# Performance work log

Measured on AMD Instinct MI355X. Metric: run time of the kernel, lower is better.

The kernel has to match this reference:

```python
import jax, jax.numpy as jnp
import numpy as np

NUM_HEADS = 16
HEAD_DIM = 64
ROT_DIM = HEAD_DIM // 2  # RotaryEmbedding(dim=head_dim/2) rotates first 32 dims only
THETA = 10000.0


def _rope(x):
    # x: [b, h, l, d]; interleaved (lucidrains) rotary on first ROT_DIM dims.
    L = x.shape[-2]
    inv_freq = 1.0 / (THETA ** (jnp.arange(0, ROT_DIM, 2, dtype=jnp.float32) / ROT_DIM))  # [ROT_DIM/2]
    ang = jnp.arange(L, dtype=jnp.float32)[:, None] * inv_freq[None, :]  # [l, ROT_DIM/2]
    ang = jnp.repeat(ang, 2, axis=-1)  # [l, ROT_DIM] (each freq repeated for the pair)
    cos, sin = jnp.cos(ang), jnp.sin(ang)
    x_rot, x_pass = x[..., :ROT_DIM], x[..., ROT_DIM:]
    x1 = x_rot[..., 0::2]
    x2 = x_rot[..., 1::2]
    rot_half = jnp.stack([-x2, x1], axis=-1).reshape(x_rot.shape)  # rotate_half, interleaved
    x_rot = x_rot * cos + rot_half * sin
    return jnp.concatenate([x_rot, x_pass], axis=-1)


def setup_inputs() -> dict:
    key = jax.random.key(0)
    ks = jax.random.split(key, 7)
    B, L, E = 2, 2048, 1024
    s = 1.0 / np.sqrt(E)
    return {
        "query": jax.random.normal(ks[0], (B, L, E), jnp.float32),
        "key": jax.random.normal(ks[1], (B, L, E), jnp.float32),
        "value": jax.random.normal(ks[2], (B, L, E), jnp.float32),
        "Wq": jax.random.normal(ks[3], (E, E), jnp.float32) * s,
        "Wk": jax.random.normal(ks[4], (E, E), jnp.float32) * s,
        "Wv": jax.random.normal(ks[5], (E, E), jnp.float32) * s,
        "Wo": jax.random.normal(ks[6], (E, E), jnp.float32) * s,
        "bo": jnp.zeros((E,), jnp.float32),
    }


def reference(query, key, value, Wq, Wk, Wv, Wo, bo):
    B, L, E = query.shape
    H, D = NUM_HEADS, HEAD_DIM
    scaling = D ** (-0.5)

    def split_heads(x):
        return x.reshape(B, L, H, D).transpose(0, 2, 1, 3)  # b h l d

    q = split_heads(query @ Wq.T)
    k = split_heads(key @ Wk.T)
    v = split_heads(value @ Wv.T)
    q = _rope(q)
    k = _rope(k)
    # NOTE: source divides by scaling (multiplies by sqrt(D)) -- faithful to original.
    attn_weight = jnp.einsum('bhid,bhjd->bhij', q, k) / scaling
    # NOTE: softmax over dim=-2 (query axis), as in the original code.
    attn_weight = jax.nn.softmax(attn_weight, axis=-2)
    attn = jnp.einsum('bhij,bhjd->bhid', attn_weight, v)
    attn = attn.transpose(0, 2, 1, 3).reshape(B, L, E)
    out = attn @ Wo.T + bo
    return out, attn_weight
```

## Files before the change

kernel.cpp:

```cpp
#include <hip/hip_runtime.h>
#include <cmath>

typedef __bf16 bf16;
typedef __attribute__((ext_vector_type(4))) __bf16 bf16x4;
typedef __attribute__((ext_vector_type(8))) __bf16 bf16x8;
typedef __attribute__((ext_vector_type(4))) float f32x4;

#define MFMA16(a, b, c) __builtin_amdgcn_mfma_f32_16x16x32_bf16((a), (b), (c), 0, 0, 0)
#define SETPRIO1 __builtin_amdgcn_s_setprio(1)
#define SETPRIO0 __builtin_amdgcn_s_setprio(0)
#define EXP2(x) __builtin_amdgcn_exp2f(x)
#define WAITV_BAR(N) asm volatile("s_waitcnt vmcnt(" #N ")\n\ts_barrier" ::: "memory")
#define WAITL_BAR    asm volatile("s_waitcnt lgkmcnt(0)\n\ts_barrier" ::: "memory")

#define LOG2E 1.4426950408889634f

static __device__ __forceinline__ void gload16(const bf16* g, bf16* l)
{
  __builtin_amdgcn_global_load_lds((const __attribute__((address_space(1))) void*)g,
                                   (__attribute__((address_space(3))) void*)l, 16, 0, 0);
}

static __device__ __forceinline__ void split4(const float4 v, bf16x4& h, bf16x4& l)
{
  h[0] = (bf16)v.x; l[0] = (bf16)(v.x - (float)h[0]);
  h[1] = (bf16)v.y; l[1] = (bf16)(v.y - (float)h[1]);
  h[2] = (bf16)v.z; l[2] = (bf16)(v.z - (float)h[2]);
  h[3] = (bf16)v.w; l[3] = (bf16)(v.w - (float)h[3]);
}

__global__ __launch_bounds__(256) void conv_kernel(
    const float* __restrict__ query, const float* __restrict__ key, const float* __restrict__ value,
    const float* __restrict__ Wq, const float* __restrict__ Wk, const float* __restrict__ Wv,
    const float* __restrict__ Wo,
    bf16* __restrict__ qh, bf16* __restrict__ ql, bf16* __restrict__ kh, bf16* __restrict__ kl,
    bf16* __restrict__ wqh, bf16* __restrict__ wql, bf16* __restrict__ wkh, bf16* __restrict__ wkl,
    bf16* __restrict__ vb, bf16* __restrict__ wvb, bf16* __restrict__ wob)
{
  const int i = blockIdx.x * 256 + threadIdx.x;
  const float* src;
  bf16 *dh, *dl;
  int e;
  if (i < 1048576)      { src = query; dh = qh; dl = ql; e = i; }
  else if (i < 2097152) { src = key;   dh = kh; dl = kl; e = i - 1048576; }
  else if (i < 3145728) { src = value; dh = vb; dl = nullptr; e = i - 2097152; }
  else {
    const int w = i - 3145728;
    const int which = w >> 18;
    e = w & 262143;
    src = (which == 0) ? Wq : (which == 1) ? Wk : (which == 2) ? Wv : Wo;
    dh  = (which == 0) ? wqh : (which == 1) ? wkh : (which == 2) ? wvb : wob;
    dl  = (which == 0) ? wql : (which == 1) ? wkl : nullptr;
  }
  const float4 v = ((const float4*)src)[e];
  bf16x4 h, l;
  split4(v, h, l);
  *(bf16x4*)(dh + (size_t)e * 4) = h;
  if (dl) *(bf16x4*)(dl + (size_t)e * 4) = l;
}

__global__ __launch_bounds__(256) void projqk_kernel(
    const bf16* __restrict__ qh, const bf16* __restrict__ ql,
    const bf16* __restrict__ kh, const bf16* __restrict__ kl,
    const bf16* __restrict__ wqh, const bf16* __restrict__ wql,
    const bf16* __restrict__ wkh, const bf16* __restrict__ wkl,
    bf16* __restrict__ Qh_g, bf16* __restrict__ Ql_g,
    bf16* __restrict__ Kh_g, bf16* __restrict__ Kl_g)
{
  const int which = blockIdx.y;
  const bf16* ta[4];
  ta[0] = which ? kh : qh;   ta[1] = which ? kl : ql;
  ta[2] = which ? wkh : wqh; ta[3] = which ? wkl : wql;
  bf16* oh = which ? Kh_g : Qh_g;
  bf16* ol = which ? Kl_g : Ql_g;
  const float oscale = which ? 8.0f * LOG2E : 1.0f;

  __shared__ __align__(16) bf16 sm[2][4][4096];
  const int tid = threadIdx.x, lane = tid & 63, w = tid >> 6;
  const int wm = w >> 1, wn = w & 1;
  const int fr = lane & 15, fg = lane >> 4;
  const int bm = blockIdx.x >> 3, bn = blockIdx.x & 7;
  const int rb[4] = {bm * 128, bm * 128, bn * 128, bn * 128};
  const int lrow = lane >> 2, lcol = (lane & 3) * 8;

  auto stage = [&](int buf, int kt) {
#pragma unroll
    for (int tl = 0; tl < 4; ++tl)
#pragma unroll
      for (int q = 0; q < 2; ++q) {
        const int r = (q * 4 + w) * 16 + lrow;
        gload16(ta[tl] + (size_t)(rb[tl] + r) * 1024 + kt * 32 + lcol,
                &sm[buf][tl][(q * 4 + w) * 512]);
      }
  };

  f32x4 acc[4][4] = {};
  stage(0, 0);
  for (int kt = 0; kt < 32; ++kt) {
    const int cur = kt & 1;
    if (kt < 31) { stage(cur ^ 1, kt + 1); WAITV_BAR(8); }
    else         { WAITV_BAR(0); }
    bf16x8 afh[4], afl[4], bfh[4], bfl[4];
#pragma unroll
    for (int m = 0; m < 4; ++m) {
      afh[m] = *(bf16x8*)&sm[cur][0][(wm * 64 + m * 16 + fr) * 32 + fg * 8];
      afl[m] = *(bf16x8*)&sm[cur][1][(wm * 64 + m * 16 + fr) * 32 + fg * 8];
    }
#pragma unroll
    for (int n = 0; n < 4; ++n) {
      bfh[n] = *(bf16x8*)&sm[cur][2][(wn * 64 + n * 16 + fr) * 32 + fg * 8];
      bfl[n] = *(bf16x8*)&sm[cur][3][(wn * 64 + n * 16 + fr) * 32 + fg * 8];
    }
    SETPRIO1;
#pragma unroll
    for (int m = 0; m < 4; ++m)
#pragma unroll
      for (int n = 0; n < 4; ++n) {
        acc[m][n] = MFMA16(afh[m], bfh[n], acc[m][n]);
        acc[m][n] = MFMA16(afh[m], bfl[n], acc[m][n]);
        acc[m][n] = MFMA16(afl[m], bfh[n], acc[m][n]);
      }
    SETPRIO0;
    WAITL_BAR;
  }
#pragma unroll
  for (int n = 0; n < 4; ++n) {
    const int d = n * 16 + fr;
    const bool rot = (n < 2);
    const float invf = rot ? exp2f((float)(d >> 1) * (-0.83048202372184059f)) : 0.0f;
    const int odd = d & 1;
    const int col = bn * 128 + wn * 64 + n * 16 + fr;
#pragma unroll
    for (int m = 0; m < 4; ++m)
#pragma unroll
      for (int r4 = 0; r4 < 4; ++r4) {
        const int row = bm * 128 + wm * 64 + m * 16 + fg * 4 + r4;
        float x = acc[m][n][r4];
        const float p = __shfl_xor(x, 1);
        if (rot) {
          float sn, cs;
          sincosf((float)(row & 2047) * invf, &sn, &cs);
          x = odd ? x * cs + p * sn : x * cs - p * sn;
        }
        x *= oscale;
        const bf16 hv = (bf16)x;
        oh[(size_t)row * 1024 + col] = hv;
        ol[(size_t)row * 1024 + col] = (bf16)(x - (float)hv);
      }
  }
}

__global__ __launch_bounds__(256) void projv_kernel(const bf16* __restrict__ vb,
                                                    const bf16* __restrict__ wvb,
                                                    bf16* __restrict__ Vt_g)
{
  __shared__ __align__(16) bf16 sm[2][2][4096];
  const int tid = threadIdx.x, lane = tid & 63, w = tid >> 6;
  const int wm = w >> 1, wn = w & 1;
  const int fr = lane & 15, fg = lane >> 4;
  const int bm = blockIdx.x >> 3, bn = blockIdx.x & 7;
  const int lrow = lane >> 2, lcol = (lane & 3) * 8;

  auto stage = [&](int buf, int kt) {
#pragma unroll
    for (int q = 0; q < 2; ++q) {
      const int r = (q * 4 + w) * 16 + lrow;
      gload16(vb  + (size_t)(bm * 128 + r) * 1024 + kt * 32 + lcol, &sm[buf][0][(q * 4 + w) * 512]);
      gload16(wvb + (size_t)(bn * 128 + r) * 1024 + kt * 32 + lcol, &sm[buf][1][(q * 4 + w) * 512]);
    }
  };

  f32x4 acc[4][4] = {};
  stage(0, 0);
  for (int kt = 0; kt < 32; ++kt) {
    const int cur = kt & 1;
    if (kt < 31) { stage(cur ^ 1, kt + 1); WAITV_BAR(4); }
    else         { WAITV_BAR(0); }
    bf16x8 af[4], bf[4];
#pragma unroll
    for (int m = 0; m < 4; ++m) af[m] = *(bf16x8*)&sm[cur][0][(wm * 64 + m * 16 + fr) * 32 + fg * 8];
#pragma unroll
    for (int n = 0; n < 4; ++n) bf[n] = *(bf16x8*)&sm[cur][1][(wn * 64 + n * 16 + fr) * 32 + fg * 8];
    SETPRIO1;
#pragma unroll
    for (int m = 0; m < 4; ++m)
#pragma unroll
      for (int n = 0; n < 4; ++n) acc[m][n] = MFMA16(af[m], bf[n], acc[m][n]);
    SETPRIO0;
    WAITL_BAR;
  }
#pragma unroll
  for (int m = 0; m < 4; ++m) {
    const int row0 = bm * 128 + wm * 64 + m * 16 + fg * 4;
    const int b = row0 >> 11, l0 = row0 & 2047;
#pragma unroll
    for (int n = 0; n < 4; ++n) {
      const int col = bn * 128 + wn * 64 + n * 16 + fr;
      const int h = col >> 6, d = col & 63;
      bf16x4 pk;
#pragma unroll
      for (int j = 0; j < 4; ++j) pk[j] = (bf16)acc[m][n][j];
      *(bf16x4*)(Vt_g + ((size_t)((b * 16 + h) * 64 + d)) * 2048 + l0) = pk;
    }
  }
}

__global__ __launch_bounds__(256) void out_kernel(const bf16* __restrict__ attnb,
                                                  const bf16* __restrict__ wob,
                                                  const float* __restrict__ bo,
                                                  float* __restrict__ out)
{
  __shared__ __align__(16) bf16 sm[2][2][4096];
  const int tid = threadIdx.x, lane = tid & 63, w = tid >> 6;
  const int wm = w >> 1, wn = w & 1;
  const int fr = lane & 15, fg = lane >> 4;
  const int bm = blockIdx.x >> 3, bn = blockIdx.x & 7;
  const int lrow = lane >> 2, lcol = (lane & 3) * 8;

  auto stage = [&](int buf, int kt) {
#pragma unroll
    for (int q = 0; q < 2; ++q) {
      const int r = (q * 4 + w) * 16 + lrow;
      gload16(attnb + (size_t)(bm * 128 + r) * 1024 + kt * 32 + lcol, &sm[buf][0][(q * 4 + w) * 512]);
      gload16(wob   + (size_t)(bn * 128 + r) * 1024 + kt * 32 + lcol, &sm[buf][1][(q * 4 + w) * 512]);
    }
  };

  f32x4 acc[4][4] = {};
  stage(0, 0);
  for (int kt = 0; kt < 32; ++kt) {
    const int cur = kt & 1;
    if (kt < 31) { stage(cur ^ 1, kt + 1); WAITV_BAR(4); }
    else         { WAITV_BAR(0); }
    bf16x8 af[4], bf[4];
#pragma unroll
    for (int m = 0; m < 4; ++m) af[m] = *(bf16x8*)&sm[cur][0][(wm * 64 + m * 16 + fr) * 32 + fg * 8];
#pragma unroll
    for (int n = 0; n < 4; ++n) bf[n] = *(bf16x8*)&sm[cur][1][(wn * 64 + n * 16 + fr) * 32 + fg * 8];
    SETPRIO1;
#pragma unroll
    for (int m = 0; m < 4; ++m)
#pragma unroll
      for (int n = 0; n < 4; ++n) acc[m][n] = MFMA16(af[m], bf[n], acc[m][n]);
    SETPRIO0;
    WAITL_BAR;
  }
#pragma unroll
  for (int m = 0; m < 4; ++m)
#pragma unroll
    for (int n = 0; n < 4; ++n) {
      const int col = bn * 128 + wn * 64 + n * 16 + fr;
      const float bv = bo[col];
#pragma unroll
      for (int r4 = 0; r4 < 4; ++r4) {
        const int row = bm * 128 + wm * 64 + m * 16 + fg * 4 + r4;
        out[(size_t)row * 1024 + col] = acc[m][n][r4] + bv;
      }
    }
}

__global__ __launch_bounds__(512) void stats_kernel(const bf16* __restrict__ Qh_g, const bf16* __restrict__ Ql_g,
                                                    const bf16* __restrict__ Kh_g, const bf16* __restrict__ Kl_g,
                                                    float* __restrict__ colmax, float* __restrict__ csuminv)
{
  __shared__ __align__(16) bf16 smh[2][8192], sml[2][8192];
  const int swz = (blockIdx.x & 7) * 64 + (blockIdx.x >> 3);
  const int bh = swz >> 4, jb = swz & 15;
  const int b = bh >> 4, h = bh & 15;
  const int t = threadIdx.x, lane = t & 63, w = t >> 6;
  const int fr = lane & 15, fg = lane >> 4;
  const int lr = lane >> 3, lc = lane & 7;

  auto stageQ = [&](int buf, int it) {
#pragma unroll
    for (int q = 0; q < 2; ++q) {
      const int r = (q * 8 + w) * 8 + lr;
      const size_t g = (size_t)(b * 2048 + it * 128 + r) * 1024 + h * 64 + ((lc ^ (r & 7)) * 8);
      gload16(Qh_g + g, &smh[buf][(q * 8 + w) * 512]);
      gload16(Ql_g + g, &sml[buf][(q * 8 + w) * 512]);
    }
  };

#pragma unroll
  for (int q = 0; q < 2; ++q) {
    const int r = (q * 8 + w) * 8 + lr;
    const size_t g = (size_t)(b * 2048 + jb * 128 + r) * 1024 + h * 64 + ((lc ^ (r & 7)) * 8);
    gload16(Kh_g + g, &smh[1][(q * 8 + w) * 512]);
    gload16(Kl_g + g, &sml[1][(q * 8 + w) * 512]);
  }
  stageQ(0, 0);
  WAITV_BAR(4);
  bf16x8 kfh[2], kfl[2];
#pragma unroll
  for (int ks = 0; ks < 2; ++ks) {
    const int rr = w * 16 + fr;
    const int cc = (ks * 32 + fg * 8) ^ ((rr & 7) << 3);
    kfh[ks] = *(bf16x8*)&smh[1][rr * 64 + cc];
    kfl[ks] = *(bf16x8*)&sml[1][rr * 64 + cc];
  }
  WAITL_BAR;

  float rm[4] = {-1e30f, -1e30f, -1e30f, -1e30f};
  float rs[4] = {0.f, 0.f, 0.f, 0.f};
  for (int it = 0; it < 16; ++it) {
    const int cur = it & 1;
    if (it < 15) { stageQ(cur ^ 1, it + 1); WAITV_BAR(4); }
    else         { WAITV_BAR(0); }
    f32x4 acc[8] = {};
    SETPRIO1;
#pragma unroll
    for (int ks = 0; ks < 2; ++ks)
#pragma unroll
      for (int n = 0; n < 8; ++n) {
        const int rr = n * 16 + fr;
        const int cc = (ks * 32 + fg * 8) ^ ((rr & 7) << 3);
        const bf16x8 qf = *(bf16x8*)&smh[cur][rr * 64 + cc];
        const bf16x8 lf = *(bf16x8*)&sml[cur][rr * 64 + cc];
        acc[n] = MFMA16(kfh[ks], qf, acc[n]);
        acc[n] = MFMA16(kfh[ks], lf, acc[n]);
        acc[n] = MFMA16(kfl[ks], qf, acc[n]);
      }
    SETPRIO0;
#pragma unroll
    for (int r4 = 0; r4 < 4; ++r4) {
      const float m = fmaxf(fmaxf(fmaxf(acc[0][r4], acc[1][r4]), fmaxf(acc[2][r4], acc[3][r4])),
                            fmaxf(fmaxf(acc[4][r4], acc[5][r4]), fmaxf(acc[6][r4], acc[7][r4])));
      const float mn = fmaxf(rm[r4], m);
      float ts = 0.f;
#pragma unroll
      for (int n = 0; n < 8; ++n) ts += EXP2(acc[n][r4] - mn);
      rs[r4] = rs[r4] * EXP2(rm[r4] - mn) + ts;
      rm[r4] = mn;
    }
    WAITL_BAR;
  }
#pragma unroll
  for (int r4 = 0; r4 < 4; ++r4) {
    float M = rm[r4];
#pragma unroll
    for (int off = 1; off < 16; off <<= 1) M = fmaxf(M, __shfl_xor(M, off));
    float s = rs[r4] * EXP2(rm[r4] - M);
#pragma unroll
    for (int off = 1; off < 16; off <<= 1) s += __shfl_xor(s, off);
    rm[r4] = M;
    rs[r4] = s;
  }
  if (fr == 0) {
#pragma unroll
    for (int r4 = 0; r4 < 4; ++r4) {
      const int j = jb * 128 + w * 16 + fg * 4 + r4;
      colmax[bh * 2048 + j] = rm[r4];
      csuminv[bh * 2048 + j] = 1.0f / rs[r4];
    }
  }
}

__global__ __launch_bounds__(256) void attn_kernel(const bf16* __restrict__ Qh_g, const bf16* __restrict__ Ql_g,
                                                   const bf16* __restrict__ Kh_g, const bf16* __restrict__ Kl_g,
                                                   const bf16* __restrict__ Vt_g,
                                                   const float* __restrict__ colmax, const float* __restrict__ csuminv,
                                                   float* __restrict__ P, bf16* __restrict__ attnb)
{
  __shared__ __align__(16) unsigned char smem[46080];
  bf16(*Kh)[72] = (bf16(*)[72])smem;
  bf16(*Kl)[72] = (bf16(*)[72])(smem + 9216);
  bf16(*Vt)[72] = (bf16(*)[72])(smem + 18432);
  bf16(*Pb)[72] = (bf16(*)[72])(smem + 27648);
  bf16(*Qh)[72] = (bf16(*)[72])smem;
  bf16(*Ql)[72] = (bf16(*)[72])(smem + 18432);

  const int swz = (blockIdx.x & 7) * 64 + (blockIdx.x >> 3);
  const int bh = swz >> 4, ib = swz & 15;
  const int b = bh >> 4, h = bh & 15;
  const int t = threadIdx.x, lane = t & 63, w = t >> 6;
  const int fr = lane & 15, fg = lane >> 4;

#pragma unroll
  for (int q = 0; q < 4; ++q) {
    const int u = q * 256 + t, r = u >> 3, c8 = (u & 7) * 8;
    const size_t g = (size_t)(b * 2048 + ib * 128 + r) * 1024 + h * 64 + c8;
    *(bf16x8*)&Qh[r][c8] = *(const bf16x8*)(Qh_g + g);
    *(bf16x8*)&Ql[r][c8] = *(const bf16x8*)(Ql_g + g);
  }
  WAITL_BAR;
  bf16x8 qfh[2][2], qfl[2][2];
#pragma unroll
  for (int mf = 0; mf < 2; ++mf)
#pragma unroll
    for (int ks = 0; ks < 2; ++ks) {
      qfh[mf][ks] = *(bf16x8*)&Qh[w * 32 + mf * 16 + fr][ks * 32 + fg * 8];
      qfl[mf][ks] = *(bf16x8*)&Ql[w * 32 + mf * 16 + fr][ks * 32 + fg * 8];
    }

  bf16x8 rKh[2], rKl[2], rV[2];
  auto loadT = [&](int jt1) {
#pragma unroll
    for (int q = 0; q < 2; ++q) {
      const int u = q * 256 + t, r = u >> 3, c8 = (u & 7) * 8;
      const size_t g = (size_t)(b * 2048 + jt1 * 64 + r) * 1024 + h * 64 + c8;
      rKh[q] = *(const bf16x8*)(Kh_g + g);
      rKl[q] = *(const bf16x8*)(Kl_g + g);
      rV[q]  = *(const bf16x8*)(Vt_g + (size_t)(bh * 64 + r) * 2048 + jt1 * 64 + c8);
    }
  };
  auto writeK = [&]() {
#pragma unroll
    for (int q = 0; q < 2; ++q) {
      const int u = q * 256 + t, r = u >> 3, c8 = (u & 7) * 8;
      *(bf16x8*)&Kh[r][c8] = rKh[q];
      *(bf16x8*)&Kl[r][c8] = rKl[q];
    }
  };
  auto writeV = [&]() {
#pragma unroll
    for (int q = 0; q < 2; ++q) {
      const int u = q * 256 + t, r = u >> 3, c8 = (u & 7) * 8;
      *(bf16x8*)&Vt[r][c8] = rV[q];
    }
  };

  loadT(0);
  WAITL_BAR;
  writeK(); writeV();
  WAITL_BAR;

  f32x4 oacc[2][4] = {};
  for (int jt = 0; jt < 32; ++jt) {
    if (jt < 31) loadT(jt + 1);
    float cmr[4], rcr[4];
#pragma unroll
    for (int nj = 0; nj < 4; ++nj) {
      const int jg = jt * 64 + nj * 16 + fr;
      cmr[nj] = colmax[bh * 2048 + jg];
      rcr[nj] = csuminv[bh * 2048 + jg];
    }
    f32x4 s[2][4] = {};
    SETPRIO1;
#pragma unroll
    for (int ks = 0; ks < 2; ++ks)
#pragma unroll
      for (int nj = 0; nj < 4; ++nj) {
        const bf16x8 khf = *(bf16x8*)&Kh[nj * 16 + fr][ks * 32 + fg * 8];
        const bf16x8 klf = *(bf16x8*)&Kl[nj * 16 + fr][ks * 32 + fg * 8];
#pragma unroll
        for (int mf = 0; mf < 2; ++mf) {
          s[mf][nj] = MFMA16(qfh[mf][ks], khf, s[mf][nj]);
          s[mf][nj] = MFMA16(qfh[mf][ks], klf, s[mf][nj]);
          s[mf][nj] = MFMA16(qfl[mf][ks], khf, s[mf][nj]);
        }
      }
    SETPRIO0;
#pragma unroll
    for (int nj = 0; nj < 4; ++nj)
#pragma unroll
      for (int mf = 0; mf < 2; ++mf)
#pragma unroll
        for (int r4 = 0; r4 < 4; ++r4) {
          const int il = w * 32 + mf * 16 + fg * 4 + r4;
          const float pv = EXP2(s[mf][nj][r4] - cmr[nj]) * rcr[nj];
          s[mf][nj][r4] = pv;
          Pb[il][nj * 16 + fr] = (bf16)pv;
        }
    WAITL_BAR;
    if (jt < 31) writeK();
#pragma unroll
    for (int nj = 0; nj < 4; ++nj) {
      const int jg = jt * 64 + nj * 16 + fr;
#pragma unroll
      for (int mf = 0; mf < 2; ++mf)
#pragma unroll
        for (int r4 = 0; r4 < 4; ++r4) {
          const int il = w * 32 + mf * 16 + fg * 4 + r4;
          P[(size_t)(bh * 2048 + ib * 128 + il) * 2048 + jg] = s[mf][nj][r4];
        }
    }
    SETPRIO1;
#pragma unroll
    for (int ks = 0; ks < 2; ++ks) {
      bf16x8 pa[2];
#pragma unroll
      for (int mf = 0; mf < 2; ++mf) pa[mf] = *(bf16x8*)&Pb[w * 32 + mf * 16 + fr][ks * 32 + fg * 8];
#pragma unroll
      for (int nd = 0; nd < 4; ++nd) {
        const bf16x8 vbf = *(bf16x8*)&Vt[nd * 16 + fr][ks * 32 + fg * 8];
#pragma unroll
        for (int mf = 0; mf < 2; ++mf) oacc[mf][nd] = MFMA16(pa[mf], vbf, oacc[mf][nd]);
      }
    }
    SETPRIO0;
    WAITL_BAR;
    if (jt < 31) writeV();
  }
#pragma unroll
  for (int mf = 0; mf < 2; ++mf)
#pragma unroll
    for (int nd = 0; nd < 4; ++nd)
#pragma unroll
      for (int r4 = 0; r4 < 4; ++r4) {
        const int il = ib * 128 + w * 32 + mf * 16 + fg * 4 + r4;
        attnb[(size_t)(b * 2048 + il) * 1024 + h * 64 + nd * 16 + fr] = (bf16)oacc[mf][nd][r4];
      }
}

extern "C" void kernel_launch(void* const* d_in, const int* in_sizes, int n_in,
                              void* d_out, int out_size, void* d_ws, size_t ws_size,
                              hipStream_t stream)
{
  const float* query = (const float*)d_in[0];
  const float* key   = (const float*)d_in[1];
  const float* value = (const float*)d_in[2];
  const float* Wq    = (const float*)d_in[3];
  const float* Wk    = (const float*)d_in[4];
  const float* Wv    = (const float*)d_in[5];
  const float* Wo    = (const float*)d_in[6];
  const float* bo    = (const float*)d_in[7];

  float* out = (float*)d_out;
  float* P   = out + 4194304;

  bf16* qh  = (bf16*)(P + 0);
  bf16* ql  = (bf16*)(P + 2097152);
  bf16* kh  = (bf16*)(P + 4194304);
  bf16* kl  = (bf16*)(P + 6291456);
  bf16* wqh = (bf16*)(P + 8388608);
  bf16* wql = (bf16*)(P + 8912896);
  bf16* wkh = (bf16*)(P + 9437184);
  bf16* wkl = (bf16*)(P + 9961472);
  bf16* vb  = (bf16*)(P + 10485760);
  bf16* wvb = (bf16*)(P + 12582912);

  float* ws   = (float*)d_ws;
  bf16* Qh_g  = (bf16*)(ws + 0);
  bf16* Ql_g  = (bf16*)(ws + 2097152);
  bf16* Kh_g  = (bf16*)(ws + 4194304);
  bf16* Kl_g  = (bf16*)(ws + 6291456);
  bf16* Vt_g  = (bf16*)(ws + 8388608);
  bf16* attnb = (bf16*)(ws + 10485760);
  bf16* wob   = (bf16*)(ws + 12582912);
  float* cmax = ws + 13107200;
  float* csui = ws + 13172736;

  conv_kernel<<<16384, 256, 0, stream>>>(query, key, value, Wq, Wk, Wv, Wo,
                                         qh, ql, kh, kl, wqh, wql, wkh, wkl, vb, wvb, wob);
  projqk_kernel<<<dim3(256, 2), 256, 0, stream>>>(qh, ql, kh, kl, wqh, wql, wkh, wkl,
                                                  Qh_g, Ql_g, Kh_g, Kl_g);
  projv_kernel<<<256, 256, 0, stream>>>(vb, wvb, Vt_g);
  stats_kernel<<<512, 512, 0, stream>>>(Qh_g, Ql_g, Kh_g, Kl_g, cmax, csui);
  attn_kernel<<<512, 256, 0, stream>>>(Qh_g, Ql_g, Kh_g, Kl_g, Vt_g, cmax, csui, P, attnb);
  out_kernel<<<256, 256, 0, stream>>>(attnb, wob, bo, out);
}
```

Baseline: 371.5 us.

## Merge Q/K/V projections into one launch; async double-buffered K/V staging in attention

The V projection becomes a third blockIdx.y slice of a combined projection kernel, which removes one launch and lets the V tiles run alongside the Q/K tiles. In the attention kernel, the register-staged K/V loads with separate LDS writes are replaced by direct global-to-LDS loads into two XOR-swizzled buffers. The next tile is prefetched while the current one is computed. This costs more LDS per block (which may lower occupancy), and the combined kernel reserves the larger shared-memory footprint even for V blocks.

```diff
diff --git a/kernel.cpp b/kernel.cpp
--- a/kernel.cpp
+++ b/kernel.cpp
@@ -10,6 +10,7 @@
 #define SETPRIO1 __builtin_amdgcn_s_setprio(1)
 #define SETPRIO0 __builtin_amdgcn_s_setprio(0)
 #define EXP2(x) __builtin_amdgcn_exp2f(x)
+#define SCHEDBAR __builtin_amdgcn_sched_barrier(0)
 #define WAITV_BAR(N) asm volatile("s_waitcnt vmcnt(" #N ")\n\ts_barrier" ::: "memory")
 #define WAITL_BAR    asm volatile("s_waitcnt lgkmcnt(0)\n\ts_barrier" ::: "memory")
 
@@ -59,29 +60,76 @@
   if (dl) *(bf16x4*)(dl + (size_t)e * 4) = l;
 }
 
-__global__ __launch_bounds__(256) void projqk_kernel(
+__global__ __launch_bounds__(256) void proj_kernel(
     const bf16* __restrict__ qh, const bf16* __restrict__ ql,
     const bf16* __restrict__ kh, const bf16* __restrict__ kl,
     const bf16* __restrict__ wqh, const bf16* __restrict__ wql,
     const bf16* __restrict__ wkh, const bf16* __restrict__ wkl,
+    const bf16* __restrict__ vb, const bf16* __restrict__ wvb,
     bf16* __restrict__ Qh_g, bf16* __restrict__ Ql_g,
-    bf16* __restrict__ Kh_g, bf16* __restrict__ Kl_g)
-{
+    bf16* __restrict__ Kh_g, bf16* __restrict__ Kl_g,
+    bf16* __restrict__ Vt_g)
+{
+  __shared__ __align__(16) bf16 sm[2][4][4096];
+  const int tid = threadIdx.x, lane = tid & 63, w = tid >> 6;
+  const int wm = w >> 1, wn = w & 1;
+  const int fr = lane & 15, fg = lane >> 4;
+  const int bm = blockIdx.x >> 3, bn = blockIdx.x & 7;
+  const int lrow = lane >> 2, lcol = (lane & 3) * 8;
   const int which = blockIdx.y;
+
+  if (which == 2) {
+    auto stageV = [&](int buf, int kt) {
+#pragma unroll
+      for (int q = 0; q < 2; ++q) {
+        const int r = (q * 4 + w) * 16 + lrow;
+        gload16(vb  + (size_t)(bm * 128 + r) * 1024 + kt * 32 + lcol, &sm[buf][0][(q * 4 + w) * 512]);
+        gload16(wvb + (size_t)(bn * 128 + r) * 1024 + kt * 32 + lcol, &sm[buf][1][(q * 4 + w) * 512]);
+      }
+    };
+    f32x4 acc[4][4] = {};
+    stageV(0, 0);
+    for (int kt = 0; kt < 32; ++kt) {
+      const int cur = kt & 1;
+      if (kt < 31) { stageV(cur ^ 1, kt + 1); WAITV_BAR(4); }
+      else         { WAITV_BAR(0); }
+      bf16x8 af[4], bf[4];
+#pragma unroll
+      for (int m = 0; m < 4; ++m) af[m] = *(bf16x8*)&sm[cur][0][(wm * 64 + m * 16 + fr) * 32 + fg * 8];
+#pragma unroll
+      for (int n = 0; n < 4; ++n) bf[n] = *(bf16x8*)&sm[cur][1][(wn * 64 + n * 16 + fr) * 32 + fg * 8];
+      SETPRIO1;
+#pragma unroll
+      for (int m = 0; m < 4; ++m)
+#pragma unroll
+        for (int n = 0; n < 4; ++n) acc[m][n] = MFMA16(af[m], bf[n], acc[m][n]);
+      SETPRIO0;
+      WAITL_BAR;
+    }
+#pragma unroll
+    for (int m = 0; m < 4; ++m) {
+      const int row0 = bm * 128 + wm * 64 + m * 16 + fg * 4;
+      const int b = row0 >> 11, l0 = row0 & 2047;
+#pragma unroll
+      for (int n = 0; n < 4; ++n) {
+        const int col = bn * 128 + wn * 64 + n * 16 + fr;
+        const int h = col >> 6, d = col & 63;
+        bf16x4 pk;
+#pragma unroll
+        for (int j = 0; j < 4; ++j) pk[j] = (bf16)acc[m][n][j];
+        *(bf16x4*)(Vt_g + ((size_t)((b * 16 + h) * 64 + d)) * 2048 + l0) = pk;
+      }
+    }
+    return;
+  }
+
   const bf16* ta[4];
   ta[0] = which ? kh : qh;   ta[1] = which ? kl : ql;
   ta[2] = which ? wkh : wqh; ta[3] = which ? wkl : wql;
   bf16* oh = which ? Kh_g : Qh_g;
   bf16* ol = which ? Kl_g : Ql_g;
   const float oscale = which ? 8.0f * LOG2E : 1.0f;
-
-  __shared__ __align__(16) bf16 sm[2][4][4096];
-  const int tid = threadIdx.x, lane = tid & 63, w = tid >> 6;
-  const int wm = w >> 1, wn = w & 1;
-  const int fr = lane & 15, fg = lane >> 4;
-  const int bm = blockIdx.x >> 3, bn = blockIdx.x & 7;
   const int rb[4] = {bm * 128, bm * 128, bn * 128, bn * 128};
-  const int lrow = lane >> 2, lcol = (lane & 3) * 8;
 
   auto stage = [&](int buf, int kt) {
 #pragma unroll
@@ -150,61 +198,6 @@
   }
 }
 
-__global__ __launch_bounds__(256) void projv_kernel(const bf16* __restrict__ vb,
-                                                    const bf16* __restrict__ wvb,
-                                                    bf16* __restrict__ Vt_g)
-{
-  __shared__ __align__(16) bf16 sm[2][2][4096];
-  const int tid = threadIdx.x, lane = tid & 63, w = tid >> 6;
-  const int wm = w >> 1, wn = w & 1;
-  const int fr = lane & 15, fg = lane >> 4;
-  const int bm = blockIdx.x >> 3, bn = blockIdx.x & 7;
-  const int lrow = lane >> 2, lcol = (lane & 3) * 8;
-
-  auto stage = [&](int buf, int kt) {
-#pragma unroll
-    for (int q = 0; q < 2; ++q) {
-      const int r = (q * 4 + w) * 16 + lrow;
-      gload16(vb  + (size_t)(bm * 128 + r) * 1024 + kt * 32 + lcol, &sm[buf][0][(q * 4 + w) * 512]);
-      gload16(wvb + (size_t)(bn * 128 + r) * 1024 + kt * 32 + lcol, &sm[buf][1][(q * 4 + w) * 512]);
-    }
-  };
-
-  f32x4 acc[4][4] = {};
-  stage(0, 0);
-  for (int kt = 0; kt < 32; ++kt) {
-    const int cur = kt & 1;
-    if (kt < 31) { stage(cur ^ 1, kt + 1); WAITV_BAR(4); }
-    else         { WAITV_BAR(0); }
-    bf16x8 af[4], bf[4];
-#pragma unroll
-    for (int m = 0; m < 4; ++m) af[m] = *(bf16x8*)&sm[cur][0][(wm * 64 + m * 16 + fr) * 32 + fg * 8];
-#pragma unroll
-    for (int n = 0; n < 4; ++n) bf[n] = *(bf16x8*)&sm[cur][1][(wn * 64 + n * 16 + fr) * 32 + fg * 8];
-    SETPRIO1;
-#pragma unroll
-    for (int m = 0; m < 4; ++m)
-#pragma unroll
-      for (int n = 0; n < 4; ++n) acc[m][n] = MFMA16(af[m], bf[n], acc[m][n]);
-    SETPRIO0;
-    WAITL_BAR;
-  }
-#pragma unroll
-  for (int m = 0; m < 4; ++m) {
-    const int row0 = bm * 128 + wm * 64 + m * 16 + fg * 4;
-    const int b = row0 >> 11, l0 = row0 & 2047;
-#pragma unroll
-    for (int n = 0; n < 4; ++n) {
-      const int col = bn * 128 + wn * 64 + n * 16 + fr;
-      const int h = col >> 6, d = col & 63;
-      bf16x4 pk;
-#pragma unroll
-      for (int j = 0; j < 4; ++j) pk[j] = (bf16)acc[m][n][j];
-      *(bf16x4*)(Vt_g + ((size_t)((b * 16 + h) * 64 + d)) * 2048 + l0) = pk;
-    }
-  }
-}
-
 __global__ __launch_bounds__(256) void out_kernel(const bf16* __restrict__ attnb,
                                                   const bf16* __restrict__ wob,
                                                   const float* __restrict__ bo,
@@ -361,11 +354,8 @@
                                                    const float* __restrict__ colmax, const float* __restrict__ csuminv,
                                                    float* __restrict__ P, bf16* __restrict__ attnb)
 {
-  __shared__ __align__(16) unsigned char smem[46080];
-  bf16(*Kh)[72] = (bf16(*)[72])smem;
-  bf16(*Kl)[72] = (bf16(*)[72])(smem + 9216);
-  bf16(*Vt)[72] = (bf16(*)[72])(smem + 18432);
-  bf16(*Pb)[72] = (bf16(*)[72])(smem + 27648);
+  __shared__ __align__(16) unsigned char smem[67584];
+  bf16(*Pb)[72] = (bf16(*)[72])(smem + 49152);
   bf16(*Qh)[72] = (bf16(*)[72])smem;
   bf16(*Ql)[72] = (bf16(*)[72])(smem + 18432);
 
@@ -391,42 +381,30 @@
       qfh[mf][ks] = *(bf16x8*)&Qh[w * 32 + mf * 16 + fr][ks * 32 + fg * 8];
       qfl[mf][ks] = *(bf16x8*)&Ql[w * 32 + mf * 16 + fr][ks * 32 + fg * 8];
     }
-
-  bf16x8 rKh[2], rKl[2], rV[2];
-  auto loadT = [&](int jt1) {
+  WAITL_BAR;
+
+  auto stage = [&](int buf, int jt1) {
+    bf16* base = (bf16*)(smem + buf * 24576);
 #pragma unroll
     for (int q = 0; q < 2; ++q) {
-      const int u = q * 256 + t, r = u >> 3, c8 = (u & 7) * 8;
-      const size_t g = (size_t)(b * 2048 + jt1 * 64 + r) * 1024 + h * 64 + c8;
-      rKh[q] = *(const bf16x8*)(Kh_g + g);
-      rKl[q] = *(const bf16x8*)(Kl_g + g);
-      rV[q]  = *(const bf16x8*)(Vt_g + (size_t)(bh * 64 + r) * 2048 + jt1 * 64 + c8);
+      const int u = q * 256 + t, r = u >> 3, lc = u & 7;
+      const int sc = (lc ^ (r & 7)) * 8;
+      const size_t gk = (size_t)(b * 2048 + jt1 * 64 + r) * 1024 + h * 64 + sc;
+      gload16(Kh_g + gk, base + u * 8);
+      gload16(Kl_g + gk, base + 4096 + u * 8);
+      gload16(Vt_g + (size_t)(bh * 64 + r) * 2048 + jt1 * 64 + sc, base + 8192 + u * 8);
     }
   };
-  auto writeK = [&]() {
-#pragma unroll
-    for (int q = 0; q < 2; ++q) {
-      const int u = q * 256 + t, r = u >> 3, c8 = (u & 7) * 8;
-      *(bf16x8*)&Kh[r][c8] = rKh[q];
-      *(bf16x8*)&Kl[r][c8] = rKl[q];
-    }
-  };
-  auto writeV = [&]() {
-#pragma unroll
-    for (int q = 0; q < 2; ++q) {
-      const int u = q * 256 + t, r = u >> 3, c8 = (u & 7) * 8;
-      *(bf16x8*)&Vt[r][c8] = rV[q];
-    }
-  };
-
-  loadT(0);
-  WAITL_BAR;
-  writeK(); writeV();
-  WAITL_BAR;
+
+  stage(0, 0);
+  WAITV_BAR(0);
 
   f32x4 oacc[2][4] = {};
   for (int jt = 0; jt < 32; ++jt) {
-    if (jt < 31) loadT(jt + 1);
+    const int cur = jt & 1;
+    bf16* bufK  = (bf16*)(smem + cur * 24576);
+    bf16* bufKl = bufK + 4096;
+    bf16* bufV  = bufK + 8192;
     float cmr[4], rcr[4];
 #pragma unroll
     for (int nj = 0; nj < 4; ++nj) {
@@ -440,8 +418,10 @@
     for (int ks = 0; ks < 2; ++ks)
 #pragma unroll
       for (int nj = 0; nj < 4; ++nj) {
-        const bf16x8 khf = *(bf16x8*)&Kh[nj * 16 + fr][ks * 32 + fg * 8];
-        const bf16x8 klf = *(bf16x8*)&Kl[nj * 16 + fr][ks * 32 + fg * 8];
+        const int rr = nj * 16 + fr;
+        const int cc = ((ks * 4 + fg) ^ (rr & 7)) * 8;
+        const bf16x8 khf = *(bf16x8*)(bufK + rr * 64 + cc);
+        const bf16x8 klf = *(bf16x8*)(bufKl + rr * 64 + cc);
 #pragma unroll
         for (int mf = 0; mf < 2; ++mf) {
           s[mf][nj] = MFMA16(qfh[mf][ks], khf, s[mf][nj]);
@@ -462,7 +442,8 @@
           Pb[il][nj * 16 + fr] = (bf16)pv;
         }
     WAITL_BAR;
-    if (jt < 31) writeK();
+    if (jt < 31) stage(cur ^ 1, jt + 1);
+    SCHEDBAR;
 #pragma unroll
     for (int nj = 0; nj < 4; ++nj) {
       const int jg = jt * 64 + nj * 16 + fr;
@@ -482,14 +463,15 @@
       for (int mf = 0; mf < 2; ++mf) pa[mf] = *(bf16x8*)&Pb[w * 32 + mf * 16 + fr][ks * 32 + fg * 8];
 #pragma unroll
       for (int nd = 0; nd < 4; ++nd) {
-        const bf16x8 vbf = *(bf16x8*)&Vt[nd * 16 + fr][ks * 32 + fg * 8];
+        const int rr = nd * 16 + fr;
+        const int cc = ((ks * 4 + fg) ^ (rr & 7)) * 8;
+        const bf16x8 vbf = *(bf16x8*)(bufV + rr * 64 + cc);
 #pragma unroll
         for (int mf = 0; mf < 2; ++mf) oacc[mf][nd] = MFMA16(pa[mf], vbf, oacc[mf][nd]);
       }
     }
     SETPRIO0;
-    WAITL_BAR;
-    if (jt < 31) writeV();
+    if (jt < 31) { WAITV_BAR(32); }
   }
 #pragma unroll
   for (int mf = 0; mf < 2; ++mf)
@@ -542,9 +524,8 @@
 
   conv_kernel<<<16384, 256, 0, stream>>>(query, key, value, Wq, Wk, Wv, Wo,
                                          qh, ql, kh, kl, wqh, wql, wkh, wkl, vb, wvb, wob);
-  projqk_kernel<<<dim3(256, 2), 256, 0, stream>>>(qh, ql, kh, kl, wqh, wql, wkh, wkl,
-                                                  Qh_g, Ql_g, Kh_g, Kl_g);
-  projv_kernel<<<256, 256, 0, stream>>>(vb, wvb, Vt_g);
+  proj_kernel<<<dim3(256, 3), 256, 0, stream>>>(qh, ql, kh, kl, wqh, wql, wkh, wkl, vb, wvb,
+                                                Qh_g, Ql_g, Kh_g, Kl_g, Vt_g);
   stats_kernel<<<512, 512, 0, stream>>>(Qh_g, Ql_g, Kh_g, Kl_g, cmax, csui);
   attn_kernel<<<512, 256, 0, stream>>>(Qh_g, Ql_g, Kh_g, Kl_g, Vt_g, cmax, csui, P, attnb);
   out_kernel<<<256, 256, 0, stream>>>(attnb, wob, bo, out);
```

New measurement: 369.7 us. Within noise of the previous version (-0.5%).
